# Kernel optimization log

Hardware: AMD Instinct MI355X
Metric: run time of the kernel (lower is better)

Reference implementation:

```python
import jax, jax.numpy as jnp
import numpy as np

N_ORDERS = 2
CHUNK = 64            # real tokens per chunk
LINEAR_ACTIVATION = False
STAB = 10000.0


def _ensure_stability(x):
    x = jnp.clip(x, -STAB, STAB)
    return jnp.nan_to_num(x, nan=0.0, posinf=STAB, neginf=-STAB)


def setup_inputs() -> dict:
    key = jax.random.key(0)
    k1, k2, k3, k4 = jax.random.split(key, 4)
    B, H, NC, D = 2, 16, 32, 128
    CT = CHUNK * N_ORDERS  # 128 virtual tokens per chunk
    s = 1.0 / np.sqrt(D)
    q_chunks = jax.random.normal(k1, (B, H, NC, CT, D), jnp.float32) * s
    W = jax.random.normal(k2, (B, H, NC, CT, D), jnp.float32) * s
    U = jax.random.normal(k3, (B, H, NC, CT, D), jnp.float32) * s
    h0 = jax.random.normal(k4, (B, H, D, D), jnp.float32) * s
    return {"q_chunks": q_chunks, "W": W, "U": U, "h0": h0}


def _gelu_norm(h):
    # h_norm/2 * gelu(2*h/h_norm, tanh) applied to chunk-boundary state
    n = jnp.linalg.norm(h, axis=-1, keepdims=True) + 1e-6
    return n / 2.0 * jax.nn.gelu(2.0 * h / n, approximate=True)


def _delta_product_scan(q_chunks, W, U, h0):
    B, H, NC, CT, D = q_chunks.shape
    C = CT // N_ORDERS

    def body(h, chunk):
        q_c, w_c, u_c = chunk  # each [B,H,CT,D]
        # virtual-token layout: token c, step s lives at index c*n_orders+s
        qs = q_c.reshape(B, H, C, N_ORDERS, D)
        ws = w_c.reshape(B, H, C, N_ORDERS, D)
        us = u_c.reshape(B, H, C, N_ORDERS, D)
        state = jnp.broadcast_to(h[:, :, None], (B, H, C, D, D))  # per-token state
        outs = []
        for step in range(N_ORDERS):
            q_s = qs[:, :, :, step]
            w_s = ws[:, :, :, step]
            u_s = us[:, :, :, step]
            k_trans_h = jnp.einsum('bhcd,bhcde->bhce', w_s, state)
            u_val = u_s - k_trans_h
            o_inter = jnp.einsum('bhcd,bhcde->bhce', q_s, state)
            o_intra = q_s * u_val  # elementwise, as in source
            outs.append(o_intra + o_inter)
            state = _ensure_stability(state + w_s[..., :, None] * u_val[..., None, :])
        out = jnp.stack(outs, axis=3).reshape(B, H, CT, D)
        h_new = state[:, :, -1]
        if not LINEAR_ACTIVATION:
            h_new = _gelu_norm(h_new)
        return h_new, out

    chunks = (jnp.moveaxis(q_chunks, 2, 0), jnp.moveaxis(W, 2, 0), jnp.moveaxis(U, 2, 0))
    h_final, ys = jax.lax.scan(body, h0, chunks)
    return jnp.moveaxis(ys, 0, 2), h_final  # [B,H,NC,CT,D], [B,H,D,D]


def reference(q_chunks, W, U, h0):
    return _delta_product_scan(q_chunks, W, U, h0)
```

## Files before the change

### kernel.cpp

```cpp
#include <hip/hip_runtime.h>


#define Dd 128
#define NCH 32
#define YS 16777216

typedef __attribute__((ext_vector_type(4))) float floatx4;
typedef __attribute__((ext_vector_type(8))) short short8;

__device__ __forceinline__ unsigned cvtpk(float lo, float hi) {
  unsigned r;
  asm("v_cvt_pk_bf16_f32 %0, %1, %2" : "=v"(r) : "v"(lo), "v"(hi));
  return r;
}

__global__ __launch_bounds__(1024, 4) void p1_scan(const float* __restrict__ W,
    const float* __restrict__ U, const float* __restrict__ h0,
    unsigned short* __restrict__ hws, float* __restrict__ out) {
  __shared__ float wpre[NCH * 320];
  __shared__ float upre[NCH * 2 * Dd];
  __shared__ float d10pre[NCH];
  __shared__ float sqb[Dd * 129];
  __shared__ float nrm2[8 * 20];

  const int bh = blockIdx.x;
  const int t = threadIdx.x;
  const int w = t >> 6, l = t & 63;
  const int cl = l & 7;
  const int c = (w << 3) | cl;
  const int rg = l >> 3;

  {
    const float* Wg = W + (size_t)bh * NCH * 16384;
    const float* Ug = U + (size_t)bh * NCH * 16384;
#pragma unroll
    for (int k = 0; k < 2; k++) {
      int idx4 = k * 1024 + t;
      int n = idx4 >> 6;
      int rem = idx4 & 63;
      int r = rem >> 5, e4 = (rem & 31) * 4;
      size_t g = (size_t)n * 16384 + (size_t)(126 + r) * Dd + e4;
      *(float4*)&upre[idx4 * 4] = *(const float4*)&Ug[g];
      *(float4*)&wpre[n * 320 + r * 160 + (e4 >> 4) * 20 + (e4 & 15)] =
          *(const float4*)&Wg[g];
    }
  }
  {
    const float4* hg = (const float4*)(h0 + (size_t)bh * 16384);
#pragma unroll
    for (int k = 0; k < 4; k++) {
      int idx4 = k * 1024 + t;
      float4 v = hg[idx4];
      int d = idx4 >> 5, e4 = (idx4 & 31) * 4;
      sqb[d * 129 + e4 + 0] = v.x;
      sqb[d * 129 + e4 + 1] = v.y;
      sqb[d * 129 + e4 + 2] = v.z;
      sqb[d * 129 + e4 + 3] = v.w;
    }
  }
  __syncthreads();
  {
    int n = t >> 5, j = t & 31;
    const float* w0p = &wpre[n * 320 + (j >> 2) * 20 + (j & 3) * 4];
    const float* w1p = w0p + 160;
    float p = 0.f;
#pragma unroll
    for (int i = 0; i < 4; i++) p += w0p[i] * w1p[i];
    p += __shfl_xor(p, 1, 64);
    p += __shfl_xor(p, 2, 64);
    p += __shfl_xor(p, 4, 64);
    p += __shfl_xor(p, 8, 64);
    p += __shfl_xor(p, 16, 64);
    if (j == 0) d10pre[n] = p;
  }
  float hr[16];
#pragma unroll
  for (int i = 0; i < 16; i++) hr[i] = sqb[(rg * 16 + i) * 129 + c];
  __syncthreads();

  const int cpos = (c & 96) | ((c + 20 * rg) & 31);
  float* sqw = &sqb[rg * 16 * 129 + cpos];
  const int srow = t >> 3, sst = t & 7;
  const float* sqr = &sqb[srow * 129 + sst * 16];

  unsigned short* hwsb = hws + (size_t)bh * NCH * 16384;
  {
    unsigned pk[8];
#pragma unroll
    for (int i = 0; i < 8; i++) pk[i] = cvtpk(hr[2 * i], hr[2 * i + 1]);
    uint4* dst = (uint4*)(hwsb + (size_t)c * Dd + rg * 16);
    dst[0] = make_uint4(pk[0], pk[1], pk[2], pk[3]);
    dst[1] = make_uint4(pk[4], pk[5], pk[6], pk[7]);
  }

  for (int n = 0; n < NCH; n++) {
    floatx4 w0v[4], w1v[4];
    const float* wb = &wpre[n * 320 + rg * 20];
#pragma unroll
    for (int i = 0; i < 4; i++) {
      w0v[i] = *(const floatx4*)&wb[4 * i];
      w1v[i] = *(const floatx4*)&wb[160 + 4 * i];
    }
    float a0 = 0.f, a1 = 0.f, b0 = 0.f, b1 = 0.f;
#pragma unroll
    for (int i = 0; i < 4; i += 2) {
#pragma unroll
      for (int j = 0; j < 4; j++) {
        float h0v = hr[4 * i + j];
        float h1v = hr[4 * i + 4 + j];
        a0 = fmaf(w0v[i][j], h0v, a0);
        a1 = fmaf(w1v[i][j], h0v, a1);
        b0 = fmaf(w0v[i + 1][j], h1v, b0);
        b1 = fmaf(w1v[i + 1][j], h1v, b1);
      }
    }
    a0 += b0; a1 += b1;
    a0 += __shfl_xor(a0, 8, 64);
    a0 += __shfl_xor(a0, 16, 64);
    a0 += __shfl_xor(a0, 32, 64);
    a1 += __shfl_xor(a1, 8, 64);
    a1 += __shfl_xor(a1, 16, 64);
    a1 += __shfl_xor(a1, 32, 64);
    const float u0 = upre[n * 256 + c];
    const float u1 = upre[n * 256 + Dd + c];
    const float d10 = d10pre[n];
    const float uv0 = u0 - a0;
    const float uv1 = u1 - a1 - d10 * uv0;
#pragma unroll
    for (int i = 0; i < 4; i++)
#pragma unroll
      for (int j = 0; j < 4; j++) {
        int ii = 4 * i + j;
        float s = __builtin_amdgcn_fmed3f(fmaf(w0v[i][j], uv0, hr[ii]),
                                          -10000.0f, 10000.0f);
        s = __builtin_amdgcn_fmed3f(fmaf(w1v[i][j], uv1, s),
                                    -10000.0f, 10000.0f);
        hr[ii] = s;
        sqw[ii * 129] = s;
      }
    __syncthreads();
    {
      float acc = 0.f, acc2 = 0.f;
#pragma unroll
      for (int b = 0; b < 4; b++) {
        const float* p = sqr + 4 * ((b + sst) & 3);
        float v0 = p[0], v1 = p[1], v2 = p[2], v3 = p[3];
        acc = fmaf(v0, v0, acc);
        acc2 = fmaf(v1, v1, acc2);
        acc = fmaf(v2, v2, acc);
        acc2 = fmaf(v3, v3, acc2);
      }
      acc += acc2;
      acc += __shfl_xor(acc, 1, 64);
      acc += __shfl_xor(acc, 2, 64);
      acc += __shfl_xor(acc, 4, 64);
      if (sst == 0) {
        float nd = sqrtf(acc) + 1e-6f;
        nrm2[(srow >> 4) * 20 + (srow & 15)] = __fdividef(2.0f, nd);
      }
    }
    __syncthreads();
    floatx4 r2v[4];
    const float* nb = &nrm2[rg * 20];
#pragma unroll
    for (int i = 0; i < 4; i++) r2v[i] = *(const floatx4*)&nb[4 * i];
#pragma unroll
    for (int i = 0; i < 4; i++)
#pragma unroll
      for (int j = 0; j < 4; j++) {
        int ii = 4 * i + j;
        float h = hr[ii];
        float x = h * r2v[i][j];
        float x2 = x * x;
        float aa = x * fmaf(0.071354816f, x2, 1.59576912f);
        float ex = __expf(-aa);
        hr[ii] = __fdividef(h, 1.0f + ex);
      }
    if (n < NCH - 1) {
      unsigned pk[8];
#pragma unroll
      for (int i = 0; i < 8; i++) pk[i] = cvtpk(hr[2 * i], hr[2 * i + 1]);
      uint4* dst = (uint4*)(hwsb + (size_t)(n + 1) * 16384 + (size_t)c * Dd + rg * 16);
      dst[0] = make_uint4(pk[0], pk[1], pk[2], pk[3]);
      dst[1] = make_uint4(pk[4], pk[5], pk[6], pk[7]);
    } else {
      float* ob = out + YS + (size_t)bh * 16384;
#pragma unroll
      for (int i = 0; i < 16; i++) ob[(rg * 16 + i) * Dd + c] = hr[i];
    }
  }
}


__device__ __forceinline__ void stage_slice(const float* Qb, const float* Wb,
    float* qd, float* wd, int kc, int wv6, int ln) {
#pragma unroll
  for (int i = 0; i < 4; i++) {
    int cb = i * 512 + wv6 * 64;
    int isW = cb >> 10;
    int cbm = cb & 1023;
    int c = cbm + ln;
    int r = c >> 3;
    int s = (c >> 4) & 7;
    const float* g = (isW ? Wb : Qb) + r * Dd + kc * 32 + (((c & 7) ^ s) << 2);
    float* l = (isW ? wd : qd) + (cbm << 2);
    __builtin_amdgcn_global_load_lds(
        (const __attribute__((address_space(1))) void*)g,
        (__attribute__((address_space(3))) void*)l, 16, 0, 0);
  }
}

__global__ __launch_bounds__(512, 4) void p2_out(const float* __restrict__ Q,
    const float* __restrict__ W, const float* __restrict__ U,
    const unsigned short* __restrict__ hws, float* __restrict__ out) {
  __shared__ unsigned short hT[Dd * 136];
  __shared__ float qsl[4096];
  __shared__ float wsl[4096];
  __shared__ float d10s[64], dq1s[64];
  __shared__ float dps[512];

  const int bid = blockIdx.x;
  const int n = bid & 31, bh = bid >> 5;
  const size_t base = (size_t)(bh * NCH + n) * 16384;
  const float* Qb = Q + base;
  const float* Wb = W + base;
  const float* Ub = U + base;
  float* Ob = out + base;
  const int t = threadIdx.x;
  const int wv6 = t >> 6, ln = t & 63;

  stage_slice(Qb, Wb, &qsl[0], &wsl[0], 0, wv6, ln);

  {
    const uint4* src = (const uint4*)(hws + base);
#pragma unroll
    for (int i = 0; i < 4; i++) {
      int idx = t + i * 512;
      uint4 v = src[idx];
      int e = idx >> 4, j = idx & 15;
      *(uint4*)&hT[e * 136 + j * 8] = v;
    }
  }
  {
    int which = t >> 8, tt = t & 255;
    int cc = tt >> 2, part = tt & 3;
    const float4* ar = (const float4*)((which ? Qb : Wb) + (2 * cc + 1) * Dd + part * 32);
    const float4* w0r = (const float4*)(Wb + (2 * cc) * Dd + part * 32);
    float s = 0.f;
#pragma unroll
    for (int i = 0; i < 8; i++) {
      float4 a = ar[i], b = w0r[i];
      s += a.x * b.x + a.y * b.y + a.z * b.z + a.w * b.w;
    }
    dps[which * 256 + tt] = s;
  }
  __syncthreads();
  if (t < 128) {
    int which = t >> 6, cc = t & 63;
    const float* p = dps + which * 256 + cc * 4;
    float s = p[0] + p[1] + p[2] + p[3];
    (which ? dq1s : d10s)[cc] = s;
  }

  const int pr = wv6 >> 2, eq = wv6 & 3;
  const int lm = ln & 15, lq = ln >> 4;
  const int sw = lm & 7;
  const int i0 = ((2 * lq) ^ sw) << 2;
  const int i1 = ((2 * lq + 1) ^ sw) << 2;

  floatx4 acc[2][4][2];
#pragma unroll
  for (int m = 0; m < 2; m++)
#pragma unroll
    for (int ci = 0; ci < 4; ci++)
#pragma unroll
      for (int j = 0; j < 2; j++) acc[m][ci][j] = (floatx4){0.f, 0.f, 0.f, 0.f};

  for (int kc = 0; kc < 4; kc++) {
    const int k0 = kc * 32;
    short8 bfr[2];
#pragma unroll
    for (int j = 0; j < 2; j++) {
      int ee = (2 * eq + j) * 16 + lm;
      bfr[j] = *(const short8*)&hT[ee * 136 + k0 + 8 * lq];
    }
#pragma unroll
    for (int ci = 0; ci < 4; ci++) {
      const int rb = (32 * ci + 2 * lm) * 32 + pr * 32;
      {
        const float* p = &qsl[rb];
        floatx4 g0 = *(const floatx4*)(p + i0);
        floatx4 g1 = *(const floatx4*)(p + i1);
        union { short8 v; unsigned u[4]; } af;
        af.u[0] = cvtpk(g0[0], g0[1]);
        af.u[1] = cvtpk(g0[2], g0[3]);
        af.u[2] = cvtpk(g1[0], g1[1]);
        af.u[3] = cvtpk(g1[2], g1[3]);
        acc[0][ci][0] = __builtin_amdgcn_mfma_f32_16x16x32_bf16(af.v, bfr[0], acc[0][ci][0], 0, 0, 0);
        acc[0][ci][1] = __builtin_amdgcn_mfma_f32_16x16x32_bf16(af.v, bfr[1], acc[0][ci][1], 0, 0, 0);
      }
      {
        const float* p = &wsl[rb];
        floatx4 g0 = *(const floatx4*)(p + i0);
        floatx4 g1 = *(const floatx4*)(p + i1);
        union { short8 v; unsigned u[4]; } af;
        af.u[0] = cvtpk(g0[0], g0[1]);
        af.u[1] = cvtpk(g0[2], g0[3]);
        af.u[2] = cvtpk(g1[0], g1[1]);
        af.u[3] = cvtpk(g1[2], g1[3]);
        acc[1][ci][0] = __builtin_amdgcn_mfma_f32_16x16x32_bf16(af.v, bfr[0], acc[1][ci][0], 0, 0, 0);
        acc[1][ci][1] = __builtin_amdgcn_mfma_f32_16x16x32_bf16(af.v, bfr[1], acc[1][ci][1], 0, 0, 0);
      }
    }
    __syncthreads();
    if (kc < 3) {
      stage_slice(Qb, Wb, &qsl[0], &wsl[0], kc + 1, wv6, ln);
      __syncthreads();
    }
  }

  float* uv0s = (float*)hT;
  if (pr == 0) {
#pragma unroll
    for (int ci = 0; ci < 4; ci++)
#pragma unroll
      for (int j = 0; j < 2; j++) {
        int ee = (2 * eq + j) * 16 + lm;
#pragma unroll
        for (int r = 0; r < 4; r++) {
          int cc = ci * 16 + lq * 4 + r;
          float T0 = acc[1][ci][j][r];
          float Q0h = acc[0][ci][j][r];
          float u0 = Ub[(2 * cc) * Dd + ee];
          float q0 = Qb[(2 * cc) * Dd + ee];
          float uv0 = u0 - T0;
          uv0s[cc * Dd + ee] = uv0;
          Ob[(2 * cc) * Dd + ee] = q0 * uv0 + Q0h;
        }
      }
  }
  __syncthreads();
  if (pr == 1) {
#pragma unroll
    for (int ci = 0; ci < 4; ci++)
#pragma unroll
      for (int j = 0; j < 2; j++) {
        int ee = (2 * eq + j) * 16 + lm;
#pragma unroll
        for (int r = 0; r < 4; r++) {
          int cc = ci * 16 + lq * 4 + r;
          float T1 = acc[1][ci][j][r];
          float Q1h = acc[0][ci][j][r];
          float u1 = Ub[(2 * cc + 1) * Dd + ee];
          float q1 = Qb[(2 * cc + 1) * Dd + ee];
          float uv0 = uv0s[cc * Dd + ee];
          float uv1 = u1 - T1 - d10s[cc] * uv0;
          Ob[(2 * cc + 1) * Dd + ee] = q1 * uv1 + Q1h + dq1s[cc] * uv0;
        }
      }
  }
}

extern "C" void kernel_launch(void* const* d_in, const int* in_sizes, int n_in,
                              void* d_out, int out_size, void* d_ws, size_t ws_size,
                              hipStream_t stream) {
  const float* Q = (const float*)d_in[0];
  const float* W = (const float*)d_in[1];
  const float* U = (const float*)d_in[2];
  const float* h0 = (const float*)d_in[3];
  float* out = (float*)d_out;
  unsigned short* hws = (unsigned short*)d_ws;

  p1_scan<<<32, 1024, 0, stream>>>(W, U, h0, hws, out);
  p2_out<<<1024, 512, 0, stream>>>(Q, W, U, hws, out);
}
```

Before: 375.7 us.

## Double-buffer Q/W slices and read h directly from global in p2_out

In p2_out, the Q/W LDS slices are now double-buffered, so the next k-slice is prefetched while the MFMAs run on the current one, and one barrier per iteration is dropped. The bf16 state tile is no longer staged in LDS; each wave loads its B fragments straight from global memory. Work is remapped so each wave owns a 16-token group with both virtual steps and half of the output columns. This removes the LDS round-trip for uv0 and the second epilogue barrier, at the cost of more accumulator registers and uncoalesced global fragment reads of h.

New measurement: 398.3 us. 6.0% more time.

```diff
diff --git a/kernel.cpp b/kernel.cpp
--- a/kernel.cpp
+++ b/kernel.cpp
@@ -213,9 +213,8 @@
 __global__ __launch_bounds__(512, 4) void p2_out(const float* __restrict__ Q,
     const float* __restrict__ W, const float* __restrict__ U,
     const unsigned short* __restrict__ hws, float* __restrict__ out) {
-  __shared__ unsigned short hT[Dd * 136];
-  __shared__ float qsl[4096];
-  __shared__ float wsl[4096];
+  __shared__ float qsl[2][4096];
+  __shared__ float wsl[2][4096];
   __shared__ float d10s[64], dq1s[64];
   __shared__ float dps[512];
 
@@ -225,22 +224,13 @@
   const float* Qb = Q + base;
   const float* Wb = W + base;
   const float* Ub = U + base;
+  const unsigned short* Hb = hws + base;
   float* Ob = out + base;
   const int t = threadIdx.x;
   const int wv6 = t >> 6, ln = t & 63;
 
-  stage_slice(Qb, Wb, &qsl[0], &wsl[0], 0, wv6, ln);
-
-  {
-    const uint4* src = (const uint4*)(hws + base);
-#pragma unroll
-    for (int i = 0; i < 4; i++) {
-      int idx = t + i * 512;
-      uint4 v = src[idx];
-      int e = idx >> 4, j = idx & 15;
-      *(uint4*)&hT[e * 136 + j * 8] = v;
-    }
-  }
+  stage_slice(Qb, Wb, &qsl[0][0], &wsl[0][0], 0, wv6, ln);
+
   {
     int which = t >> 8, tt = t & 255;
     int cc = tt >> 2, part = tt & 3;
@@ -262,102 +252,73 @@
     (which ? dq1s : d10s)[cc] = s;
   }
 
-  const int pr = wv6 >> 2, eq = wv6 & 3;
+  const int ct = wv6 >> 1, eh = wv6 & 1;
   const int lm = ln & 15, lq = ln >> 4;
   const int sw = lm & 7;
   const int i0 = ((2 * lq) ^ sw) << 2;
   const int i1 = ((2 * lq + 1) ^ sw) << 2;
-
-  floatx4 acc[2][4][2];
-#pragma unroll
-  for (int m = 0; m < 2; m++)
-#pragma unroll
-    for (int ci = 0; ci < 4; ci++)
-#pragma unroll
-      for (int j = 0; j < 2; j++) acc[m][ci][j] = (floatx4){0.f, 0.f, 0.f, 0.f};
-
+  const int rbase = (32 * ct + 2 * lm) * 32;
+
+  floatx4 acc[4][4];
+#pragma unroll
+  for (int m = 0; m < 4; m++)
+#pragma unroll
+    for (int e = 0; e < 4; e++) acc[m][e] = (floatx4){0.f, 0.f, 0.f, 0.f};
+
+  int cur = 0;
   for (int kc = 0; kc < 4; kc++) {
+    if (kc < 3)
+      stage_slice(Qb, Wb, &qsl[cur ^ 1][0], &wsl[cur ^ 1][0], kc + 1, wv6, ln);
     const int k0 = kc * 32;
-    short8 bfr[2];
-#pragma unroll
-    for (int j = 0; j < 2; j++) {
-      int ee = (2 * eq + j) * 16 + lm;
-      bfr[j] = *(const short8*)&hT[ee * 136 + k0 + 8 * lq];
-    }
-#pragma unroll
-    for (int ci = 0; ci < 4; ci++) {
-      const int rb = (32 * ci + 2 * lm) * 32 + pr * 32;
-      {
-        const float* p = &qsl[rb];
-        floatx4 g0 = *(const floatx4*)(p + i0);
-        floatx4 g1 = *(const floatx4*)(p + i1);
-        union { short8 v; unsigned u[4]; } af;
-        af.u[0] = cvtpk(g0[0], g0[1]);
-        af.u[1] = cvtpk(g0[2], g0[3]);
-        af.u[2] = cvtpk(g1[0], g1[1]);
-        af.u[3] = cvtpk(g1[2], g1[3]);
-        acc[0][ci][0] = __builtin_amdgcn_mfma_f32_16x16x32_bf16(af.v, bfr[0], acc[0][ci][0], 0, 0, 0);
-        acc[0][ci][1] = __builtin_amdgcn_mfma_f32_16x16x32_bf16(af.v, bfr[1], acc[0][ci][1], 0, 0, 0);
-      }
-      {
-        const float* p = &wsl[rb];
-        floatx4 g0 = *(const floatx4*)(p + i0);
-        floatx4 g1 = *(const floatx4*)(p + i1);
-        union { short8 v; unsigned u[4]; } af;
-        af.u[0] = cvtpk(g0[0], g0[1]);
-        af.u[1] = cvtpk(g0[2], g0[3]);
-        af.u[2] = cvtpk(g1[0], g1[1]);
-        af.u[3] = cvtpk(g1[2], g1[3]);
-        acc[1][ci][0] = __builtin_amdgcn_mfma_f32_16x16x32_bf16(af.v, bfr[0], acc[1][ci][0], 0, 0, 0);
-        acc[1][ci][1] = __builtin_amdgcn_mfma_f32_16x16x32_bf16(af.v, bfr[1], acc[1][ci][1], 0, 0, 0);
-      }
-    }
+    short8 bfr[4];
+#pragma unroll
+    for (int e = 0; e < 4; e++) {
+      int ee = (eh * 4 + e) * 16 + lm;
+      bfr[e] = *(const short8*)&Hb[ee * Dd + k0 + 8 * lq];
+    }
+    const float* qp = &qsl[cur][rbase];
+    const float* wp = &wsl[cur][rbase];
+    short8 am[4];
+#pragma unroll
+    for (int m = 0; m < 4; m++) {
+      const float* p = (m < 2 ? qp : wp) + (m & 1) * 32;
+      floatx4 g0 = *(const floatx4*)(p + i0);
+      floatx4 g1 = *(const floatx4*)(p + i1);
+      union { short8 v; unsigned u[4]; } af;
+      af.u[0] = cvtpk(g0[0], g0[1]);
+      af.u[1] = cvtpk(g0[2], g0[3]);
+      af.u[2] = cvtpk(g1[0], g1[1]);
+      af.u[3] = cvtpk(g1[2], g1[3]);
+      am[m] = af.v;
+    }
+#pragma unroll
+    for (int m = 0; m < 4; m++)
+#pragma unroll
+      for (int e = 0; e < 4; e++)
+        acc[m][e] = __builtin_amdgcn_mfma_f32_16x16x32_bf16(am[m], bfr[e], acc[m][e], 0, 0, 0);
     __syncthreads();
-    if (kc < 3) {
-      stage_slice(Qb, Wb, &qsl[0], &wsl[0], kc + 1, wv6, ln);
-      __syncthreads();
-    }
-  }
-
-  float* uv0s = (float*)hT;
-  if (pr == 0) {
-#pragma unroll
-    for (int ci = 0; ci < 4; ci++)
-#pragma unroll
-      for (int j = 0; j < 2; j++) {
-        int ee = (2 * eq + j) * 16 + lm;
-#pragma unroll
-        for (int r = 0; r < 4; r++) {
-          int cc = ci * 16 + lq * 4 + r;
-          float T0 = acc[1][ci][j][r];
-          float Q0h = acc[0][ci][j][r];
-          float u0 = Ub[(2 * cc) * Dd + ee];
-          float q0 = Qb[(2 * cc) * Dd + ee];
-          float uv0 = u0 - T0;
-          uv0s[cc * Dd + ee] = uv0;
-          Ob[(2 * cc) * Dd + ee] = q0 * uv0 + Q0h;
-        }
-      }
-  }
-  __syncthreads();
-  if (pr == 1) {
-#pragma unroll
-    for (int ci = 0; ci < 4; ci++)
-#pragma unroll
-      for (int j = 0; j < 2; j++) {
-        int ee = (2 * eq + j) * 16 + lm;
-#pragma unroll
-        for (int r = 0; r < 4; r++) {
-          int cc = ci * 16 + lq * 4 + r;
-          float T1 = acc[1][ci][j][r];
-          float Q1h = acc[0][ci][j][r];
-          float u1 = Ub[(2 * cc + 1) * Dd + ee];
-          float q1 = Qb[(2 * cc + 1) * Dd + ee];
-          float uv0 = uv0s[cc * Dd + ee];
-          float uv1 = u1 - T1 - d10s[cc] * uv0;
-          Ob[(2 * cc + 1) * Dd + ee] = q1 * uv1 + Q1h + dq1s[cc] * uv0;
-        }
-      }
+    cur ^= 1;
+  }
+
+#pragma unroll
+  for (int e = 0; e < 4; e++) {
+    int ee = (eh * 4 + e) * 16 + lm;
+#pragma unroll
+    for (int r = 0; r < 4; r++) {
+      int cc = ct * 16 + lq * 4 + r;
+      float Q0h = acc[0][e][r];
+      float Q1h = acc[1][e][r];
+      float T0 = acc[2][e][r];
+      float T1 = acc[3][e][r];
+      float u0 = Ub[(2 * cc) * Dd + ee];
+      float q0 = Qb[(2 * cc) * Dd + ee];
+      float uv0 = u0 - T0;
+      Ob[(2 * cc) * Dd + ee] = q0 * uv0 + Q0h;
+      float u1 = Ub[(2 * cc + 1) * Dd + ee];
+      float q1 = Qb[(2 * cc + 1) * Dd + ee];
+      float uv1 = u1 - T1 - d10s[cc] * uv0;
+      Ob[(2 * cc + 1) * Dd + ee] = q1 * uv1 + Q1h + dq1s[cc] * uv0;
+    }
   }
 }
 
```
